# Optimization experiments

Measured on AMD Instinct MI355X. Metric: run time of the kernel, lower is better.

Reference implementation:

```python
import jax, jax.numpy as jnp
import numpy as np

K = 3          # kernel_size
EPS = 1e-12    # epsilon from l2_normal and abs-clamp


def setup_inputs() -> dict:
    key = jax.random.key(0)
    k1, k2 = jax.random.split(key)
    B, H, W, C, F = 8, 224, 224, 32, 32
    image = jax.random.normal(k1, (B, H, W, C), dtype=jnp.float32)
    # glorot-uniform-ish weight, shape (1, C*K*K, filters)
    fan = C * K * K + F
    lim = np.sqrt(6.0 / fan).astype(np.float32)
    w = jax.random.uniform(k2, (1, C * K * K, F), dtype=jnp.float32, minval=-lim, maxval=lim)
    p = jnp.full((F,), 100.0 ** 0.5, dtype=jnp.float32)   # p init = sqrt(100)
    q = jnp.full((1,), 10.0 ** 0.5, dtype=jnp.float32)    # q init = sqrt(10)
    return {"image": image, "w": w, "p": p, "q": q}


def reference(image, w, p, q):
    # CosSim2D, kernel_size=3, stride=1, padding='same', non-depthwise.
    B, H, W, C = image.shape
    pad = K // 2
    padded = jnp.pad(image, ((0, 0), (pad, pad), (pad, pad), (0, 0)))
    # im2col: kernel-position-major, channel-minor -> matches tf.stack(axis=3) + reshape
    patches = jnp.stack(
        [padded[:, dy:dy + H, dx:dx + W, :] for dy in range(K) for dx in range(K)],
        axis=3,
    )  # (B, H, W, K*K, C)
    x = patches.reshape(B, H * W, K * K * C)
    q_term = jnp.square(q) / 10.0                       # scalar (broadcast)
    x_norm = jnp.sqrt(jnp.maximum(jnp.sum(x * x, axis=2, keepdims=True), EPS)) + q_term
    w_norm = jnp.sqrt(jnp.maximum(jnp.sum(w * w, axis=1, keepdims=True), EPS)) + q_term
    sim = jnp.matmul(x / x_norm, (w / w_norm)[0])       # (B, H*W, filters)
    out = jnp.sign(sim) * jnp.power(jnp.abs(sim) + EPS, jnp.square(p) / 100.0)
    return out.reshape(B, H, W, -1)
```

## Files before the change

### kernel.cpp

```cpp
#include <hip/hip_runtime.h>
#include <hip/hip_bf16.h>


#define H_ 224
#define W_ 224
#define C_ 32
#define F_ 32

#define NSTEP 18
#define HROWS 10
#define HCOLS 34

typedef __bf16 bf16_t;
typedef bf16_t bf16x8 __attribute__((ext_vector_type(8)));
typedef float f32x16 __attribute__((ext_vector_type(16)));

#define WFRAG_BYTES (NSTEP * 64 * 8 * 2)

__global__ __launch_bounds__(256) void cos2d_prep(
    const float* __restrict__ w, const float* __restrict__ p,
    const float* __restrict__ q, bf16_t* __restrict__ wfrag,
    float* __restrict__ winv, float* __restrict__ ef) {
  __shared__ float part[8][32];
  const int tid = threadIdx.x;
  const int f = tid & 31, kg = tid >> 5;
  float s = 0.f;
#pragma unroll
  for (int i = 0; i < 36; ++i) {
    const float v = w[(kg + 8 * i) * F_ + f];
    s += v * v;
  }
  part[kg][f] = s;
  __syncthreads();
  if (tid < 32) {
    float t = 0.f;
#pragma unroll
    for (int g = 0; g < 8; ++g) t += part[g][tid];
    const float qt = q[0] * q[0] * 0.1f;
    winv[tid] = 1.f / (sqrtf(fmaxf(t, 1e-12f)) + qt);
    ef[tid] = p[tid] * p[tid] * 0.01f;
  }
  for (int t = tid; t < NSTEP * 64; t += 256) {
    const int s2 = t >> 6, l = t & 63;
    const int ff = l & 31;
    union { bf16_t v[8]; uint4 u; } tv;
#pragma unroll
    for (int e = 0; e < 8; ++e) {
      const int kk = s2 * 16 + ((l >> 5) << 3) + e;
      tv.v[e] = (bf16_t)w[kk * F_ + ff];
    }
    *(uint4*)(wfrag + (size_t)t * 8) = tv.u;
  }
}

__global__ __launch_bounds__(256, 5) void cos2d_main(
    const float* __restrict__ img, const bf16_t* __restrict__ wfrag,
    const float* __restrict__ winv, const float* __restrict__ ef,
    const float* __restrict__ q, float* __restrict__ out) {
  __shared__ bf16_t xt[HROWS][HCOLS][40];
  __shared__ float ssum[HROWS][HCOLS];

  const int tid = threadIdx.x;
  const int lane = tid & 63;
  const int wv = tid >> 6;
  const int lp = lane & 31;

  const int bid = blockIdx.x;
  const int tw = bid % 7;
  const int th = (bid / 7) % 28;
  const int b  = bid / 196;
  const int h0 = th * 8, w0 = tw * 32;

  const float qt = q[0] * q[0] * 0.1f;
  const float efv = ef[lp];
  const float wnv = winv[lp];

  for (int idx = tid; idx < HROWS * HCOLS; idx += 256) {
    const int rr = idx / HCOLS, cc = idx - rr * HCOLS;
    const int hh = h0 - 1 + rr, wc = w0 - 1 + cc;
    float s = 0.f;
    union { bf16_t v[32]; uint4 u[4]; } tv;
    if ((unsigned)hh < H_ && (unsigned)wc < W_) {
      const float4* p4 =
          (const float4*)(img + ((size_t)(b * H_ + hh) * W_ + wc) * C_);
#pragma unroll
      for (int jj = 0; jj < 8; ++jj) {
        const float4 v = p4[jj];
        s += v.x * v.x + v.y * v.y + v.z * v.z + v.w * v.w;
        tv.v[4 * jj + 0] = (bf16_t)v.x;
        tv.v[4 * jj + 1] = (bf16_t)v.y;
        tv.v[4 * jj + 2] = (bf16_t)v.z;
        tv.v[4 * jj + 3] = (bf16_t)v.w;
      }
    } else {
#pragma unroll
      for (int jj = 0; jj < 4; ++jj) tv.u[jj] = make_uint4(0u, 0u, 0u, 0u);
    }
    ssum[rr][cc] = s;
    uint4* dst = (uint4*)&xt[rr][cc][0];
#pragma unroll
    for (int jj = 0; jj < 4; ++jj) dst[jj] = tv.u[jj];
  }
  __syncthreads();

  const int mr0 = wv * 2;

  float xinv[2];
#pragma unroll
  for (int t = 0; t < 2; ++t) {
    const int mr = mr0 + t;
    const float xn2 = ssum[mr + 0][lp] + ssum[mr + 0][lp + 1] + ssum[mr + 0][lp + 2]
                    + ssum[mr + 1][lp] + ssum[mr + 1][lp + 1] + ssum[mr + 1][lp + 2]
                    + ssum[mr + 2][lp] + ssum[mr + 2][lp + 1] + ssum[mr + 2][lp + 2];
    xinv[t] = 1.f / (sqrtf(fmaxf(xn2, 1e-12f)) + qt);
  }

  f32x16 acc0, acc1;
#pragma unroll
  for (int i = 0; i < 16; ++i) { acc0[i] = 0.f; acc1[i] = 0.f; }

  const bf16x8* wf4 = (const bf16x8*)wfrag;
#pragma unroll
  for (int s2 = 0; s2 < NSTEP; ++s2) {
    const bf16x8 bf = wf4[s2 * 64 + lane];
    const int pos = s2 >> 1;
    const int dy = pos / 3, dx = pos - dy * 3;
    const int chof = (s2 & 1) * 16 + ((lane >> 5) << 3);
    const bf16x8 a0 = *(const bf16x8*)&xt[mr0 + 0 + dy][lp + dx][chof];
    const bf16x8 a1 = *(const bf16x8*)&xt[mr0 + 1 + dy][lp + dx][chof];
    acc0 = __builtin_amdgcn_mfma_f32_32x32x16_bf16(a0, bf, acc0, 0, 0, 0);
    acc1 = __builtin_amdgcn_mfma_f32_32x32x16_bf16(a1, bf, acc1, 0, 0, 0);
  }

#pragma unroll
  for (int t = 0; t < 2; ++t) {
    const f32x16& acc = t ? acc1 : acc0;
    const int obase = (b * H_ + h0 + mr0 + t) * W_ + w0;
#pragma unroll
    for (int jj = 0; jj < 16; ++jj) {
      const int row = (jj & 3) + 8 * (jj >> 2) + 4 * (lane >> 5);
      const float xi = __shfl(xinv[t], row);
      const float sim = acc[jj] * xi * wnv;
      const float ps = fabsf(sim) + 1e-12f;
      float r = exp2f(efv * __log2f(ps));
      r = copysignf(r, sim);
      out[(size_t)(obase + row) * F_ + lp] = r;
    }
  }
}

extern "C" void kernel_launch(void* const* d_in, const int* in_sizes, int n_in,
                              void* d_out, int out_size, void* d_ws, size_t ws_size,
                              hipStream_t stream) {
  const float* img = (const float*)d_in[0];
  const float* w   = (const float*)d_in[1];
  const float* p   = (const float*)d_in[2];
  const float* q   = (const float*)d_in[3];

  bf16_t* wfrag = (bf16_t*)d_ws;
  float*  winv  = (float*)((char*)d_ws + WFRAG_BYTES);
  float*  ef    = winv + 64;

  cos2d_prep<<<1, 256, 0, stream>>>(w, p, q, wfrag, winv, ef);
  cos2d_main<<<1568, 256, 0, stream>>>(img, wfrag, winv, ef, q, (float*)d_out);
}
```

Baseline: 35.89 us.

## Split halo tile loads across 8 lanes per pixel and prefetch weight fragments

The halo load now assigns eight threads per pixel, each loading one float4. Neighbouring lanes therefore read contiguous memory (coalesced), and the squared-norm is reduced with xor shuffles instead of one thread looping over 32 channels. All 18 weight fragments are loaded into registers before the tile load, so their latency overlaps it and the MFMA loop no longer waits on global reads. This raises register pressure, so launch bounds drop from 5 to 4 blocks per SM, which may reduce occupancy.

Result: slower. 37.77 us (+5.2%).

```diff
diff --git a/kernel.cpp b/kernel.cpp
--- a/kernel.cpp
+++ b/kernel.cpp
@@ -53,7 +53,7 @@
   }
 }
 
-__global__ __launch_bounds__(256, 5) void cos2d_main(
+__global__ __launch_bounds__(256, 4) void cos2d_main(
     const float* __restrict__ img, const bf16_t* __restrict__ wfrag,
     const float* __restrict__ winv, const float* __restrict__ ef,
     const float* __restrict__ q, float* __restrict__ out) {
@@ -75,31 +75,27 @@
   const float efv = ef[lp];
   const float wnv = winv[lp];
 
-  for (int idx = tid; idx < HROWS * HCOLS; idx += 256) {
-    const int rr = idx / HCOLS, cc = idx - rr * HCOLS;
+  bf16x8 bfrag[NSTEP];
+  const bf16x8* wf4 = (const bf16x8*)wfrag;
+#pragma unroll
+  for (int s2 = 0; s2 < NSTEP; ++s2) bfrag[s2] = wf4[s2 * 64 + lane];
+
+  for (int idx = tid; idx < HROWS * HCOLS * 8; idx += 256) {
+    const int p = idx >> 3, sub = idx & 7;
+    const int rr = p / HCOLS, cc = p - rr * HCOLS;
     const int hh = h0 - 1 + rr, wc = w0 - 1 + cc;
-    float s = 0.f;
-    union { bf16_t v[32]; uint4 u[4]; } tv;
-    if ((unsigned)hh < H_ && (unsigned)wc < W_) {
-      const float4* p4 =
-          (const float4*)(img + ((size_t)(b * H_ + hh) * W_ + wc) * C_);
-#pragma unroll
-      for (int jj = 0; jj < 8; ++jj) {
-        const float4 v = p4[jj];
-        s += v.x * v.x + v.y * v.y + v.z * v.z + v.w * v.w;
-        tv.v[4 * jj + 0] = (bf16_t)v.x;
-        tv.v[4 * jj + 1] = (bf16_t)v.y;
-        tv.v[4 * jj + 2] = (bf16_t)v.z;
-        tv.v[4 * jj + 3] = (bf16_t)v.w;
-      }
-    } else {
-#pragma unroll
-      for (int jj = 0; jj < 4; ++jj) tv.u[jj] = make_uint4(0u, 0u, 0u, 0u);
-    }
-    ssum[rr][cc] = s;
-    uint4* dst = (uint4*)&xt[rr][cc][0];
-#pragma unroll
-    for (int jj = 0; jj < 4; ++jj) dst[jj] = tv.u[jj];
+    float4 v = make_float4(0.f, 0.f, 0.f, 0.f);
+    if ((unsigned)hh < H_ && (unsigned)wc < W_)
+      v = *(const float4*)(img + ((size_t)(b * H_ + hh) * W_ + wc) * C_ + sub * 4);
+    float s = v.x * v.x + v.y * v.y + v.z * v.z + v.w * v.w;
+    s += __shfl_xor(s, 1);
+    s += __shfl_xor(s, 2);
+    s += __shfl_xor(s, 4);
+    union { bf16_t h[4]; uint2 u; } pk;
+    pk.h[0] = (bf16_t)v.x; pk.h[1] = (bf16_t)v.y;
+    pk.h[2] = (bf16_t)v.z; pk.h[3] = (bf16_t)v.w;
+    *(uint2*)&xt[rr][cc][sub * 4] = pk.u;
+    if (sub == 0) ssum[rr][cc] = s;
   }
   __syncthreads();
 
@@ -119,17 +115,15 @@
 #pragma unroll
   for (int i = 0; i < 16; ++i) { acc0[i] = 0.f; acc1[i] = 0.f; }
 
-  const bf16x8* wf4 = (const bf16x8*)wfrag;
 #pragma unroll
   for (int s2 = 0; s2 < NSTEP; ++s2) {
-    const bf16x8 bf = wf4[s2 * 64 + lane];
     const int pos = s2 >> 1;
     const int dy = pos / 3, dx = pos - dy * 3;
     const int chof = (s2 & 1) * 16 + ((lane >> 5) << 3);
     const bf16x8 a0 = *(const bf16x8*)&xt[mr0 + 0 + dy][lp + dx][chof];
     const bf16x8 a1 = *(const bf16x8*)&xt[mr0 + 1 + dy][lp + dx][chof];
-    acc0 = __builtin_amdgcn_mfma_f32_32x32x16_bf16(a0, bf, acc0, 0, 0, 0);
-    acc1 = __builtin_amdgcn_mfma_f32_32x32x16_bf16(a1, bf, acc1, 0, 0, 0);
+    acc0 = __builtin_amdgcn_mfma_f32_32x32x16_bf16(a0, bfrag[s2], acc0, 0, 0, 0);
+    acc1 = __builtin_amdgcn_mfma_f32_32x32x16_bf16(a1, bfrag[s2], acc1, 0, 0, 0);
   }
 
 #pragma unroll
```
